# Kernel optimization log

Hardware: AMD Instinct MI355X
Metric: run time of the kernel (lower is better)

## Reference

```python
import jax, jax.numpy as jnp
import numpy as np

B, S, H, QS, VS = 32, 2048, 1024, 1024, 2048


def setup_inputs() -> dict:
    key = jax.random.key(0)
    k1, k2, k3, k4, k5, k6 = jax.random.split(key, 6)
    query = jax.random.normal(k1, (B, QS), dtype=jnp.float32)
    proj_key = jax.random.normal(k2, (B, S, H), dtype=jnp.float32)
    value = jax.random.normal(k3, (B, S, VS), dtype=jnp.float32)
    mask = jax.random.randint(k4, (B, 1, S), 0, 2, dtype=jnp.int32)
    Wq = jax.random.normal(k5, (QS, H), dtype=jnp.float32) * (1.0 / np.sqrt(QS))
    v_energy = jax.random.normal(k6, (H,), dtype=jnp.float32) * (1.0 / np.sqrt(H))
    return {"query": query, "proj_key": proj_key, "value": value,
            "mask": mask, "Wq": Wq, "v_energy": v_energy}


def reference(query, proj_key, value, mask, Wq, v_energy):
    # query_layer: [B, QS] @ [QS, H] -> [B, H], then unsqueeze to [B, 1, H]
    q = (query @ Wq)[:, None, :]
    # energy: v . tanh(q + proj_key) -> scores [B, S] -> [B, 1, S]
    scores = jnp.einsum('bsh,h->bs', jnp.tanh(q + proj_key), v_energy)[:, None, :]
    scores = jnp.where(mask == 0, -jnp.inf, scores)
    alphas = jax.nn.softmax(scores, axis=-1)            # [B, 1, S]
    context = jnp.einsum('bts,sv->btv', alphas[0:0], value[0:0]) if False else jnp.matmul(alphas, value)  # [B, 1, VS]
    return (context, alphas)
```

## Files before the change

### kernel.cpp

```cpp
#include <hip/hip_runtime.h>
#include <math.h>

#define Bb 32
#define Ss 2048
#define Hh 1024
#define QSq 1024
#define VSv 2048
#define SCH 32
#define NV 2

__device__ __forceinline__ float fast_tanh(float x) {
    float xc = fminf(fmaxf(x, -10.f), 10.f);
    float e  = __expf(2.f * xc);
    return 1.f - 2.f * __builtin_amdgcn_rcpf(e + 1.f);
}

__global__ void k_qproj(const float* __restrict__ query,
                        const float* __restrict__ Wq,
                        float* __restrict__ q) {
    __shared__ float qrow[QSq];
    const int b   = blockIdx.x >> 2;
    const int h0  = (blockIdx.x & 3) * 256;
    const int tid = threadIdx.x;
    for (int i = tid; i < QSq; i += 256) qrow[i] = query[b * QSq + i];
    __syncthreads();
    const int h = h0 + tid;
    float a0 = 0.f, a1 = 0.f, a2 = 0.f, a3 = 0.f;
#pragma unroll 8
    for (int qs = 0; qs < QSq; qs += 4) {
        a0 += qrow[qs + 0] * Wq[(size_t)(qs + 0) * Hh + h];
        a1 += qrow[qs + 1] * Wq[(size_t)(qs + 1) * Hh + h];
        a2 += qrow[qs + 2] * Wq[(size_t)(qs + 2) * Hh + h];
        a3 += qrow[qs + 3] * Wq[(size_t)(qs + 3) * Hh + h];
    }
    q[b * Hh + h] = (a0 + a1) + (a2 + a3);
}

__device__ __forceinline__ float dot_tanh4(const float* sh_q, const float* sh_v,
                                           int h, float4 p) {
    const float4 qv = *(const float4*)&sh_q[h];
    const float4 vv = *(const float4*)&sh_v[h];
    float a;
    a  = vv.x * fast_tanh(qv.x + p.x);
    a += vv.y * fast_tanh(qv.y + p.y);
    a += vv.z * fast_tanh(qv.z + p.z);
    a += vv.w * fast_tanh(qv.w + p.w);
    return a;
}

__global__ void k_scores(const float* __restrict__ pk,
                         const int*   __restrict__ mask,
                         const float* __restrict__ q,
                         const float* __restrict__ ve,
                         float* __restrict__ scores) {
    __shared__ float sh_q[Hh];
    __shared__ float sh_v[Hh];
    const int tid = threadIdx.x;
    const int b   = blockIdx.x / (Ss / 8);
    const int s0  = (blockIdx.x % (Ss / 8)) * 8;
    for (int i = tid; i < Hh; i += 256) { sh_q[i] = q[b * Hh + i]; sh_v[i] = ve[i]; }
    __syncthreads();
    const int wave = tid >> 6, lane = tid & 63;
    const int s = s0 + wave * 2;
    const int m0 = mask[b * Ss + s], m1 = mask[b * Ss + s + 1];
    if (lane == 0) {
        if (!m0) scores[b * Ss + s]     = -INFINITY;
        if (!m1) scores[b * Ss + s + 1] = -INFINITY;
    }
    if (!m0 && !m1) return;
    const float4* r0 = (const float4*)(pk + (size_t)(b * Ss + s) * Hh);
    const float4* r1 = r0 + Hh / 4;
    float acc0 = 0.f, acc1 = 0.f;
    if (m0 && m1) {
        float4 P0[4], P1[4];
#pragma unroll
        for (int j = 0; j < 4; ++j) P0[j] = r0[j * 64 + lane];
#pragma unroll
        for (int j = 0; j < 4; ++j) P1[j] = r1[j * 64 + lane];
#pragma unroll
        for (int j = 0; j < 4; ++j) {
            const int h = (j * 64 + lane) * 4;
            acc0 += dot_tanh4(sh_q, sh_v, h, P0[j]);
            acc1 += dot_tanh4(sh_q, sh_v, h, P1[j]);
        }
    } else {
        const float4* r = m0 ? r0 : r1;
        float4 P[4];
#pragma unroll
        for (int j = 0; j < 4; ++j) P[j] = r[j * 64 + lane];
        float acc = 0.f;
#pragma unroll
        for (int j = 0; j < 4; ++j) {
            const int h = (j * 64 + lane) * 4;
            acc += dot_tanh4(sh_q, sh_v, h, P[j]);
        }
        if (m0) acc0 = acc; else acc1 = acc;
    }
#pragma unroll
    for (int off = 32; off; off >>= 1) {
        acc0 += __shfl_xor(acc0, off);
        acc1 += __shfl_xor(acc1, off);
    }
    if (lane == 0) {
        if (m0) scores[b * Ss + s]     = acc0;
        if (m1) scores[b * Ss + s + 1] = acc1;
    }
}

__global__ void k_softmax(const float* __restrict__ scores,
                          float* __restrict__ alphas,
                          int*   __restrict__ lidx,
                          float* __restrict__ lal,
                          int*   __restrict__ lcount) {
    const int b = blockIdx.x, tid = threadIdx.x;
    const int wave = tid >> 6, lane = tid & 63;
    __shared__ float sred[4];
    __shared__ int   cnt[256];
    float v[8];
    float m = -INFINITY;
#pragma unroll
    for (int i = 0; i < 8; ++i) {
        v[i] = scores[b * Ss + tid * 8 + i];
        m = fmaxf(m, v[i]);
    }
#pragma unroll
    for (int off = 32; off; off >>= 1) m = fmaxf(m, __shfl_xor(m, off));
    if (lane == 0) sred[wave] = m;
    __syncthreads();
    m = fmaxf(fmaxf(sred[0], sred[1]), fmaxf(sred[2], sred[3]));
    __syncthreads();
    float e[8];
    float sum = 0.f;
#pragma unroll
    for (int i = 0; i < 8; ++i) { e[i] = __expf(v[i] - m); sum += e[i]; }
#pragma unroll
    for (int off = 32; off; off >>= 1) sum += __shfl_xor(sum, off);
    if (lane == 0) sred[wave] = sum;
    __syncthreads();
    sum = (sred[0] + sred[1]) + (sred[2] + sred[3]);
    const float inv = 1.f / sum;
#pragma unroll
    for (int i = 0; i < 8; ++i) alphas[b * Ss + tid * 8 + i] = e[i] * inv;

    int c = 0;
#pragma unroll
    for (int i = 0; i < 8; ++i) c += (v[i] > -INFINITY) ? 1 : 0;
    cnt[tid] = c;
    __syncthreads();
    for (int off = 1; off < 256; off <<= 1) {
        int add = (tid >= off) ? cnt[tid - off] : 0;
        __syncthreads();
        cnt[tid] += add;
        __syncthreads();
    }
    int pos = cnt[tid] - c;
#pragma unroll
    for (int i = 0; i < 8; ++i) {
        if (v[i] > -INFINITY) {
            lidx[b * Ss + pos] = tid * 8 + i;
            lal[b * Ss + pos]  = e[i] * inv;
            ++pos;
        }
    }
    if (tid == 255) lcount[b] = cnt[255];
}

__global__ void k_ctx_partial(const float* __restrict__ value,
                              const int*   __restrict__ lidx,
                              const float* __restrict__ lal,
                              const int*   __restrict__ lcount,
                              float* __restrict__ part) {
    __shared__ int   sidx[128];
    __shared__ float sal[128];
    const int tid  = threadIdx.x;
    const int blk  = blockIdx.x;
    const int b    = blk / (NV * SCH);
    const int rest = blk % (NV * SCH);
    const int vc   = rest / SCH;
    const int sc   = rest % SCH;
    const int v0   = vc * 1024 + tid * 4;
    const int count = lcount[b];
    const int chunk = (count + SCH - 1) / SCH;
    const int beg = sc * chunk;
    const int end = min(beg + chunk, count);
    const int n   = end - beg;
    if (tid < n) {
        sidx[tid] = lidx[b * Ss + beg + tid];
        sal[tid]  = lal[b * Ss + beg + tid];
    }
    __syncthreads();
    const float* vb = value + (size_t)b * Ss * VSv + v0;
    float4 acc0 = {0.f, 0.f, 0.f, 0.f};
    float4 acc1 = {0.f, 0.f, 0.f, 0.f};
    int i = 0;
    for (; i + 8 <= n; i += 8) {
        float4 w[8];
        float  a[8];
#pragma unroll
        for (int k = 0; k < 8; ++k) {
            w[k] = *(const float4*)(vb + (size_t)sidx[i + k] * VSv);
            a[k] = sal[i + k];
        }
#pragma unroll
        for (int k = 0; k < 8; k += 2) {
            acc0.x += a[k] * w[k].x;     acc0.y += a[k] * w[k].y;
            acc0.z += a[k] * w[k].z;     acc0.w += a[k] * w[k].w;
            acc1.x += a[k+1] * w[k+1].x; acc1.y += a[k+1] * w[k+1].y;
            acc1.z += a[k+1] * w[k+1].z; acc1.w += a[k+1] * w[k+1].w;
        }
    }
    for (; i < n; ++i) {
        const float a = sal[i];
        const float4 w = *(const float4*)(vb + (size_t)sidx[i] * VSv);
        acc0.x += a * w.x; acc0.y += a * w.y; acc0.z += a * w.z; acc0.w += a * w.w;
    }
    acc0.x += acc1.x; acc0.y += acc1.y; acc0.z += acc1.z; acc0.w += acc1.w;
    *(float4*)(part + ((size_t)(b * SCH + sc)) * VSv + v0) = acc0;
}

__global__ void k_ctx_reduce(const float* __restrict__ part,
                             float* __restrict__ out) {
    const int idx = blockIdx.x * 256 + threadIdx.x;
    const int b = idx / VSv, v = idx % VSv;
    float acc = 0.f;
#pragma unroll
    for (int c = 0; c < SCH; ++c) acc += part[((size_t)(b * SCH + c)) * VSv + v];
    out[idx] = acc;
}

extern "C" void kernel_launch(void* const* d_in, const int* in_sizes, int n_in,
                              void* d_out, int out_size, void* d_ws, size_t ws_size,
                              hipStream_t stream) {
    const float* query    = (const float*)d_in[0];
    const float* proj_key = (const float*)d_in[1];
    const float* value    = (const float*)d_in[2];
    const int*   mask     = (const int*)d_in[3];
    const float* Wq       = (const float*)d_in[4];
    const float* v_energy = (const float*)d_in[5];

    float* out        = (float*)d_out;
    float* ctx_out    = out;
    float* alphas_out = out + Bb * VSv;

    float* ws     = (float*)d_ws;
    float* q      = ws;
    float* scores = q + Bb * Hh;
    float* lal    = scores + Bb * Ss;
    int*   lidx   = (int*)(lal + Bb * Ss);
    int*   lcount = lidx + Bb * Ss;
    float* part   = (float*)(lcount + 32);

    hipLaunchKernelGGL(k_qproj,       dim3(Bb * 4),            dim3(256), 0, stream, query, Wq, q);
    hipLaunchKernelGGL(k_scores,      dim3(Bb * (Ss / 8)),     dim3(256), 0, stream, proj_key, mask, q, v_energy, scores);
    hipLaunchKernelGGL(k_softmax,     dim3(Bb),                dim3(256), 0, stream, scores, alphas_out, lidx, lal, lcount);
    hipLaunchKernelGGL(k_ctx_partial, dim3(Bb * NV * SCH),     dim3(256), 0, stream, value, lidx, lal, lcount, part);
    hipLaunchKernelGGL(k_ctx_reduce,  dim3((Bb * VSv) / 256),  dim3(256), 0, stream, part, ctx_out);
}
```

Before: 116.7 us.

## Use nontemporal streaming loads, wave-level softmax scan, and wider context blocks

Switches the proj_key and value streaming reads to nontemporal vector loads so they bypass cache retention. It replaces the softmax's block-wide LDS prefix scan with a wave shuffle scan plus a small cross-wave sum, and vectorizes the score reads and alpha stores. The context partial kernel now has each thread cover both 1024-column halves, halving the block count, and the reduce kernel works on float4. The aim is to cut cache pollution and sync overhead in the memory-bound stages, though fewer ctx blocks may lower occupancy and latency hiding.

```diff
diff --git a/kernel.cpp b/kernel.cpp
--- a/kernel.cpp
+++ b/kernel.cpp
@@ -7,12 +7,20 @@
 #define QSq 1024
 #define VSv 2048
 #define SCH 32
-#define NV 2
+
+typedef float fx4 __attribute__((ext_vector_type(4)));
 
 __device__ __forceinline__ float fast_tanh(float x) {
     float xc = fminf(fmaxf(x, -10.f), 10.f);
     float e  = __expf(2.f * xc);
     return 1.f - 2.f * __builtin_amdgcn_rcpf(e + 1.f);
+}
+
+__device__ __forceinline__ fx4 ntload4(const float* p) {
+    return __builtin_nontemporal_load((const fx4*)p);
+}
+__device__ __forceinline__ void ntstore4(float* p, fx4 v) {
+    __builtin_nontemporal_store(v, (fx4*)p);
 }
 
 __global__ void k_qproj(const float* __restrict__ query,
@@ -37,7 +45,7 @@
 }
 
 __device__ __forceinline__ float dot_tanh4(const float* sh_q, const float* sh_v,
-                                           int h, float4 p) {
+                                           int h, fx4 p) {
     const float4 qv = *(const float4*)&sh_q[h];
     const float4 vv = *(const float4*)&sh_v[h];
     float a;
@@ -68,15 +76,15 @@
         if (!m1) scores[b * Ss + s + 1] = -INFINITY;
     }
     if (!m0 && !m1) return;
-    const float4* r0 = (const float4*)(pk + (size_t)(b * Ss + s) * Hh);
-    const float4* r1 = r0 + Hh / 4;
+    const float* r0 = pk + (size_t)(b * Ss + s) * Hh;
+    const float* r1 = r0 + Hh;
     float acc0 = 0.f, acc1 = 0.f;
     if (m0 && m1) {
-        float4 P0[4], P1[4];
-#pragma unroll
-        for (int j = 0; j < 4; ++j) P0[j] = r0[j * 64 + lane];
-#pragma unroll
-        for (int j = 0; j < 4; ++j) P1[j] = r1[j * 64 + lane];
+        fx4 P0[4], P1[4];
+#pragma unroll
+        for (int j = 0; j < 4; ++j) P0[j] = ntload4(r0 + (j * 64 + lane) * 4);
+#pragma unroll
+        for (int j = 0; j < 4; ++j) P1[j] = ntload4(r1 + (j * 64 + lane) * 4);
 #pragma unroll
         for (int j = 0; j < 4; ++j) {
             const int h = (j * 64 + lane) * 4;
@@ -84,10 +92,10 @@
             acc1 += dot_tanh4(sh_q, sh_v, h, P1[j]);
         }
     } else {
-        const float4* r = m0 ? r0 : r1;
-        float4 P[4];
-#pragma unroll
-        for (int j = 0; j < 4; ++j) P[j] = r[j * 64 + lane];
+        const float* r = m0 ? r0 : r1;
+        fx4 P[4];
+#pragma unroll
+        for (int j = 0; j < 4; ++j) P[j] = ntload4(r + (j * 64 + lane) * 4);
         float acc = 0.f;
 #pragma unroll
         for (int j = 0; j < 4; ++j) {
@@ -115,54 +123,59 @@
     const int b = blockIdx.x, tid = threadIdx.x;
     const int wave = tid >> 6, lane = tid & 63;
     __shared__ float sred[4];
-    __shared__ int   cnt[256];
+    __shared__ float ssum[4];
+    __shared__ int   swt[4];
     float v[8];
+    *(float4*)&v[0] = *(const float4*)&scores[b * Ss + tid * 8];
+    *(float4*)&v[4] = *(const float4*)&scores[b * Ss + tid * 8 + 4];
     float m = -INFINITY;
 #pragma unroll
-    for (int i = 0; i < 8; ++i) {
-        v[i] = scores[b * Ss + tid * 8 + i];
-        m = fmaxf(m, v[i]);
-    }
+    for (int i = 0; i < 8; ++i) m = fmaxf(m, v[i]);
 #pragma unroll
     for (int off = 32; off; off >>= 1) m = fmaxf(m, __shfl_xor(m, off));
     if (lane == 0) sred[wave] = m;
     __syncthreads();
     m = fmaxf(fmaxf(sred[0], sred[1]), fmaxf(sred[2], sred[3]));
-    __syncthreads();
     float e[8];
     float sum = 0.f;
 #pragma unroll
     for (int i = 0; i < 8; ++i) { e[i] = __expf(v[i] - m); sum += e[i]; }
 #pragma unroll
     for (int off = 32; off; off >>= 1) sum += __shfl_xor(sum, off);
-    if (lane == 0) sred[wave] = sum;
-    __syncthreads();
-    sum = (sred[0] + sred[1]) + (sred[2] + sred[3]);
+    if (lane == 0) ssum[wave] = sum;
+    __syncthreads();
+    sum = (ssum[0] + ssum[1]) + (ssum[2] + ssum[3]);
     const float inv = 1.f / sum;
-#pragma unroll
-    for (int i = 0; i < 8; ++i) alphas[b * Ss + tid * 8 + i] = e[i] * inv;
+    float a[8];
+#pragma unroll
+    for (int i = 0; i < 8; ++i) a[i] = e[i] * inv;
+    ntstore4(&alphas[b * Ss + tid * 8],     *(fx4*)&a[0]);
+    ntstore4(&alphas[b * Ss + tid * 8 + 4], *(fx4*)&a[4]);
 
     int c = 0;
 #pragma unroll
     for (int i = 0; i < 8; ++i) c += (v[i] > -INFINITY) ? 1 : 0;
-    cnt[tid] = c;
-    __syncthreads();
-    for (int off = 1; off < 256; off <<= 1) {
-        int add = (tid >= off) ? cnt[tid - off] : 0;
-        __syncthreads();
-        cnt[tid] += add;
-        __syncthreads();
-    }
-    int pos = cnt[tid] - c;
+    int incl = c;
+#pragma unroll
+    for (int off = 1; off < 64; off <<= 1) {
+        int y = __shfl_up(incl, off);
+        if (lane >= off) incl += y;
+    }
+    if (lane == 63) swt[wave] = incl;
+    __syncthreads();
+    int base = 0;
+#pragma unroll
+    for (int w = 0; w < 4; ++w) base += (w < wave) ? swt[w] : 0;
+    int pos = base + incl - c;
 #pragma unroll
     for (int i = 0; i < 8; ++i) {
         if (v[i] > -INFINITY) {
             lidx[b * Ss + pos] = tid * 8 + i;
-            lal[b * Ss + pos]  = e[i] * inv;
+            lal[b * Ss + pos]  = a[i];
             ++pos;
         }
     }
-    if (tid == 255) lcount[b] = cnt[255];
+    if (tid == 0) lcount[b] = swt[0] + swt[1] + swt[2] + swt[3];
 }
 
 __global__ void k_ctx_partial(const float* __restrict__ value,
@@ -170,15 +183,12 @@
                               const float* __restrict__ lal,
                               const int*   __restrict__ lcount,
                               float* __restrict__ part) {
-    __shared__ int   sidx[128];
-    __shared__ float sal[128];
-    const int tid  = threadIdx.x;
-    const int blk  = blockIdx.x;
-    const int b    = blk / (NV * SCH);
-    const int rest = blk % (NV * SCH);
-    const int vc   = rest / SCH;
-    const int sc   = rest % SCH;
-    const int v0   = vc * 1024 + tid * 4;
+    __shared__ int   sidx[64];
+    __shared__ float sal[64];
+    const int tid = threadIdx.x;
+    const int b   = blockIdx.x / SCH;
+    const int sc  = blockIdx.x % SCH;
+    const int c0  = tid * 4;
     const int count = lcount[b];
     const int chunk = (count + SCH - 1) / SCH;
     const int beg = sc * chunk;
@@ -189,43 +199,47 @@
         sal[tid]  = lal[b * Ss + beg + tid];
     }
     __syncthreads();
-    const float* vb = value + (size_t)b * Ss * VSv + v0;
-    float4 acc0 = {0.f, 0.f, 0.f, 0.f};
-    float4 acc1 = {0.f, 0.f, 0.f, 0.f};
+    const float* vb = value + (size_t)b * Ss * VSv;
+    fx4 accA = {0.f, 0.f, 0.f, 0.f};
+    fx4 accB = {0.f, 0.f, 0.f, 0.f};
     int i = 0;
     for (; i + 8 <= n; i += 8) {
-        float4 w[8];
-        float  a[8];
+        fx4   wa[8], wb[8];
+        float a[8];
 #pragma unroll
         for (int k = 0; k < 8; ++k) {
-            w[k] = *(const float4*)(vb + (size_t)sidx[i + k] * VSv);
-            a[k] = sal[i + k];
-        }
-#pragma unroll
-        for (int k = 0; k < 8; k += 2) {
-            acc0.x += a[k] * w[k].x;     acc0.y += a[k] * w[k].y;
-            acc0.z += a[k] * w[k].z;     acc0.w += a[k] * w[k].w;
-            acc1.x += a[k+1] * w[k+1].x; acc1.y += a[k+1] * w[k+1].y;
-            acc1.z += a[k+1] * w[k+1].z; acc1.w += a[k+1] * w[k+1].w;
+            const float* rp = vb + (size_t)sidx[i + k] * VSv + c0;
+            wa[k] = ntload4(rp);
+            wb[k] = ntload4(rp + 1024);
+            a[k]  = sal[i + k];
+        }
+#pragma unroll
+        for (int k = 0; k < 8; ++k) {
+            accA += a[k] * wa[k];
+            accB += a[k] * wb[k];
         }
     }
     for (; i < n; ++i) {
         const float a = sal[i];
-        const float4 w = *(const float4*)(vb + (size_t)sidx[i] * VSv);
-        acc0.x += a * w.x; acc0.y += a * w.y; acc0.z += a * w.z; acc0.w += a * w.w;
-    }
-    acc0.x += acc1.x; acc0.y += acc1.y; acc0.z += acc1.z; acc0.w += acc1.w;
-    *(float4*)(part + ((size_t)(b * SCH + sc)) * VSv + v0) = acc0;
+        const float* rp = vb + (size_t)sidx[i] * VSv + c0;
+        accA += a * ntload4(rp);
+        accB += a * ntload4(rp + 1024);
+    }
+    float* pr = part + ((size_t)(b * SCH + sc)) * VSv + c0;
+    *(fx4*)pr          = accA;
+    *(fx4*)(pr + 1024) = accB;
 }
 
 __global__ void k_ctx_reduce(const float* __restrict__ part,
                              float* __restrict__ out) {
     const int idx = blockIdx.x * 256 + threadIdx.x;
-    const int b = idx / VSv, v = idx % VSv;
-    float acc = 0.f;
-#pragma unroll
-    for (int c = 0; c < SCH; ++c) acc += part[((size_t)(b * SCH + c)) * VSv + v];
-    out[idx] = acc;
+    const int b = idx / (VSv / 4), v4 = idx % (VSv / 4);
+    fx4 acc = {0.f, 0.f, 0.f, 0.f};
+#pragma unroll
+    for (int c = 0; c < SCH; ++c) {
+        acc += ntload4(part + ((size_t)(b * SCH + c)) * VSv + v4 * 4);
+    }
+    *(fx4*)(out + (size_t)b * VSv + v4 * 4) = acc;
 }
 
 extern "C" void kernel_launch(void* const* d_in, const int* in_sizes, int n_in,
@@ -250,9 +264,9 @@
     int*   lcount = lidx + Bb * Ss;
     float* part   = (float*)(lcount + 32);
 
-    hipLaunchKernelGGL(k_qproj,       dim3(Bb * 4),            dim3(256), 0, stream, query, Wq, q);
-    hipLaunchKernelGGL(k_scores,      dim3(Bb * (Ss / 8)),     dim3(256), 0, stream, proj_key, mask, q, v_energy, scores);
-    hipLaunchKernelGGL(k_softmax,     dim3(Bb),                dim3(256), 0, stream, scores, alphas_out, lidx, lal, lcount);
-    hipLaunchKernelGGL(k_ctx_partial, dim3(Bb * NV * SCH),     dim3(256), 0, stream, value, lidx, lal, lcount, part);
-    hipLaunchKernelGGL(k_ctx_reduce,  dim3((Bb * VSv) / 256),  dim3(256), 0, stream, part, ctx_out);
-}
+    hipLaunchKernelGGL(k_qproj,       dim3(Bb * 4),              dim3(256), 0, stream, query, Wq, q);
+    hipLaunchKernelGGL(k_scores,      dim3(Bb * (Ss / 8)),       dim3(256), 0, stream, proj_key, mask, q, v_energy, scores);
+    hipLaunchKernelGGL(k_softmax,     dim3(Bb),                  dim3(256), 0, stream, scores, alphas_out, lidx, lal, lcount);
+    hipLaunchKernelGGL(k_ctx_partial, dim3(Bb * SCH),            dim3(256), 0, stream, value, lidx, lal, lcount, part);
+    hipLaunchKernelGGL(k_ctx_reduce,  dim3((Bb * VSv / 4) / 256), dim3(256), 0, stream, part, ctx_out);
+}
```

New measurement: 102.4 us. 1.14x faster.
